# Kernel optimization log

Hardware: AMD Instinct MI355X
Metric: run time of the kernel (lower is better)

The kernel has to match this reference:

```python
import jax, jax.numpy as jnp
import numpy as np

D_MODEL = 1024
N_HEADS = 16
D_K = D_MODEL // N_HEADS


def setup_inputs() -> dict:
    key = jax.random.key(0)
    ks = jax.random.split(key, 11)
    B, S = 2, 2048
    s = 1.0 / np.sqrt(D_MODEL)
    return {
        "Q": jax.random.normal(ks[0], (B, S, D_MODEL), jnp.float32),
        "K": jax.random.normal(ks[1], (B, S, D_MODEL), jnp.float32),
        "V": jax.random.normal(ks[2], (B, S, D_MODEL), jnp.float32),
        "Wq": jax.random.normal(ks[3], (D_MODEL, D_MODEL), jnp.float32) * s,
        "bq": jnp.zeros((D_MODEL,), jnp.float32),
        "Wk": jax.random.normal(ks[4], (D_MODEL, D_MODEL), jnp.float32) * s,
        "bk": jnp.zeros((D_MODEL,), jnp.float32),
        "Wv": jax.random.normal(ks[5], (D_MODEL, D_MODEL), jnp.float32) * s,
        "bv": jnp.zeros((D_MODEL,), jnp.float32),
        "Wo": jax.random.normal(ks[6], (D_MODEL, D_MODEL), jnp.float32) * s,
        "bo": jnp.zeros((D_MODEL,), jnp.float32),
    }


def reference(Q, K, V, Wq, bq, Wk, bk, Wv, bv, Wo, bo):
    B, S, _ = Q.shape
    # linear projections (torch Linear: x @ W.T + b), split into heads
    def proj(x, W, b):
        y = x @ W.T + b                          # [B,S,D]
        return y.reshape(B, -1, N_HEADS, D_K).transpose(0, 2, 1, 3)  # [B,H,S,d_k]
    q = proj(Q, Wq, bq)
    k = proj(K, Wk, bk)
    v = proj(V, Wv, bv)
    scale = 1.0 / jnp.sqrt(jnp.float32(D_K))
    scores = jnp.einsum('bhqd,bhkd->bhqk', q, k) * scale  # [B,H,S,S]
    attn = jax.nn.softmax(scores, axis=-1)
    out = jnp.einsum('bhqk,bhkd->bhqd', attn, v)          # [B,H,S,d_k]
    out = out.transpose(0, 2, 1, 3).reshape(B, S, N_HEADS * D_K)
    return out @ Wo.T + bo
```

## Files before the change

kernel.cpp:

```cpp
#include <hip/hip_runtime.h>
#include <hip/hip_bf16.h>
#include <math.h>

#define D_MODEL 1024
#define NH      16
#define DK      64
#define S_LEN   2048
#define BATCH   2
#define M_ROWS  4096

typedef _Float16 f16;
typedef _Float16 f16x4 __attribute__((ext_vector_type(4)));
typedef _Float16 f16x8 __attribute__((ext_vector_type(8)));
typedef float    f32x4 __attribute__((ext_vector_type(4)));

__global__ __launch_bounds__(256) void cvt_f32_to_f16(
    const float* __restrict__ a, const float* __restrict__ b,
    const float* __restrict__ c, const float* __restrict__ d,
    f16* __restrict__ oa, f16* __restrict__ ob,
    f16* __restrict__ oc, f16* __restrict__ od, int n8) {
    const int y = blockIdx.y;
    const float* s = (y == 0) ? a : (y == 1) ? b : (y == 2) ? c : d;
    f16* o        = (y == 0) ? oa : (y == 1) ? ob : (y == 2) ? oc : od;
    if (s == nullptr) return;
    const int i = blockIdx.x * 256 + threadIdx.x;
    if (i >= n8) return;
    const size_t e = (size_t)i * 8;
    const float4 v0 = *(const float4*)&s[e];
    const float4 v1 = *(const float4*)&s[e + 4];
    f16x8 r = {(f16)v0.x, (f16)v0.y, (f16)v0.z, (f16)v0.w,
               (f16)v1.x, (f16)v1.y, (f16)v1.z, (f16)v1.w};
    *(f16x8*)&o[e] = r;
}

__device__ __forceinline__ void stage16(const f16* g, f16* l) {
    __builtin_amdgcn_global_load_lds(
        (const __attribute__((address_space(1))) unsigned int*)g,
        (__attribute__((address_space(3))) unsigned int*)l, 16, 0, 0);
}

__device__ __forceinline__ void gemm_body(const f16* __restrict__ X, const f16* __restrict__ W,
                                          const float* __restrict__ bias, void* __restrict__ Yv,
                                          const int mode, const float oscale) {
    __shared__ f16 As[128 * 32];
    __shared__ f16 Bs[128 * 32];
    const int tid = threadIdx.x;
    const int lane = tid & 63;
    const int w  = tid >> 6;
    const int wm = w >> 1, wn = w & 1;
    const int l15 = lane & 15, lhi = lane >> 4;
    const int m0 = blockIdx.y * 128, n0 = blockIdx.x * 128;

    const int srow = tid >> 2;
    const int scol = (tid & 3) * 8;

    f32x4 acc[4][4] = {};

    for (int k0 = 0; k0 < D_MODEL; k0 += 32) {
        __syncthreads();
        stage16(&X[(size_t)(m0 + srow) * D_MODEL + k0 + scol],      &As[tid * 8]);
        stage16(&X[(size_t)(m0 + 64 + srow) * D_MODEL + k0 + scol], &As[2048 + tid * 8]);
        stage16(&W[(size_t)(n0 + srow) * D_MODEL + k0 + scol],      &Bs[tid * 8]);
        stage16(&W[(size_t)(n0 + 64 + srow) * D_MODEL + k0 + scol], &Bs[2048 + tid * 8]);
        __syncthreads();
        f16x8 af[4], bf[4];
#pragma unroll
        for (int mt = 0; mt < 4; ++mt) af[mt] = *(const f16x8*)&As[(wm * 64 + mt * 16 + l15) * 32 + lhi * 8];
#pragma unroll
        for (int nt = 0; nt < 4; ++nt) bf[nt] = *(const f16x8*)&Bs[(wn * 64 + nt * 16 + l15) * 32 + lhi * 8];
#pragma unroll
        for (int mt = 0; mt < 4; ++mt)
#pragma unroll
            for (int nt = 0; nt < 4; ++nt)
                acc[mt][nt] = __builtin_amdgcn_mfma_f32_16x16x32_f16(af[mt], bf[nt], acc[mt][nt], 0, 0, 0);
    }

#pragma unroll
    for (int mt = 0; mt < 4; ++mt)
#pragma unroll
        for (int nt = 0; nt < 4; ++nt) {
            const int n = n0 + wn * 64 + nt * 16 + l15;
            const float bn = bias[n];
#pragma unroll
            for (int r = 0; r < 4; ++r) {
                const int m = m0 + wm * 64 + mt * 16 + lhi * 4 + r;
                const float v = (acc[mt][nt][r] + bn) * oscale;
                if (mode == 0) {
                    ((f16*)Yv)[((((size_t)(m >> 11) * NH + (n >> 6)) * S_LEN) + (m & 2047)) * DK + (n & 63)] = (f16)v;
                } else if (mode == 1) {
                    ((f16*)Yv)[((((size_t)(m >> 11) * NH + (n >> 6)) * DK) + (n & 63)) * S_LEN + (m & 2047)] = (f16)v;
                } else {
                    ((float*)Yv)[(size_t)m * D_MODEL + n] = v;
                }
            }
        }
}

__global__ __launch_bounds__(256) void qkv_gemm(
    const f16* __restrict__ Xq, const f16* __restrict__ Xk, const f16* __restrict__ Xv,
    const f16* __restrict__ Wq, const f16* __restrict__ Wk, const f16* __restrict__ Wv,
    const float* __restrict__ bq, const float* __restrict__ bk, const float* __restrict__ bv,
    f16* __restrict__ qh, f16* __restrict__ kh, f16* __restrict__ vt) {
    const int z = blockIdx.z;
    const f16* X = (z == 0) ? Xq : (z == 1) ? Xk : Xv;
    const f16* W = (z == 0) ? Wq : (z == 1) ? Wk : Wv;
    const float* bias = (z == 0) ? bq : (z == 1) ? bk : bv;
    f16* Y = (z == 0) ? qh : (z == 1) ? kh : vt;
    gemm_body(X, W, bias, Y, (z == 2) ? 1 : 0, (z == 0) ? 0.125f : 1.0f);
}

__global__ __launch_bounds__(256) void out_gemm(const f16* __restrict__ X, const f16* __restrict__ W,
                                                const float* __restrict__ bias, float* __restrict__ Y) {
    gemm_body(X, W, bias, Y, 2, 1.0f);
}

__global__ __launch_bounds__(256) void flash_mfma(const f16* __restrict__ qh, const f16* __restrict__ kh,
                                                  const f16* __restrict__ vt, f16* __restrict__ ao) {
    __shared__ f16 Ks[64][72];
    __shared__ f16 Vs[64][72];

    const int tid = threadIdx.x;
    const int lane = tid & 63;
    const int w = tid >> 6;
    const int c = lane & 15;
    const int g = lane >> 4;
    const int qt = blockIdx.x, bh = blockIdx.y;
    const int b = bh >> 4, h = bh & 15;
    const int qrow0 = qt * 64 + w * 16;

    f16x8 bQ0, bQ1;
    {
        const f16* qp = qh + ((size_t)bh * S_LEN + qrow0 + c) * DK;
        bQ0 = *(const f16x8*)&qp[g * 8];
        bQ1 = *(const f16x8*)&qp[32 + g * 8];
    }

    f32x4 oa[4] = {};
    float m_run = -INFINITY;
    float l_run = 0.f;

    const int cr = tid >> 3;
    const int cs = (tid & 7) * 8;

    for (int kt = 0; kt < S_LEN / 64; ++kt) {
        __syncthreads();
        {
            const uint4 k0v = *(const uint4*)&kh[((size_t)bh * S_LEN + kt * 64 + cr) * DK + cs];
            const uint4 k1v = *(const uint4*)&kh[((size_t)bh * S_LEN + kt * 64 + cr + 32) * DK + cs];
            const uint4 v0v = *(const uint4*)&vt[((size_t)bh * DK + cr) * S_LEN + kt * 64 + cs];
            const uint4 v1v = *(const uint4*)&vt[((size_t)bh * DK + cr + 32) * S_LEN + kt * 64 + cs];
            *(uint4*)&Ks[cr][cs] = k0v;
            *(uint4*)&Ks[cr + 32][cs] = k1v;
            *(uint4*)&Vs[cr][cs] = v0v;
            *(uint4*)&Vs[cr + 32][cs] = v1v;
        }
        __syncthreads();

        f32x4 sc[4] = {};
#pragma unroll
        for (int nt = 0; nt < 4; ++nt) {
            const f16x8 ka = *(const f16x8*)&Ks[nt * 16 + c][g * 8];
            const f16x8 kb = *(const f16x8*)&Ks[nt * 16 + c][32 + g * 8];
            sc[nt] = __builtin_amdgcn_mfma_f32_16x16x32_f16(ka, bQ0, sc[nt], 0, 0, 0);
            sc[nt] = __builtin_amdgcn_mfma_f32_16x16x32_f16(kb, bQ1, sc[nt], 0, 0, 0);
        }

        float tmax = sc[0][0];
#pragma unroll
        for (int nt = 0; nt < 4; ++nt)
#pragma unroll
            for (int r = 0; r < 4; ++r) tmax = fmaxf(tmax, sc[nt][r]);
        tmax = fmaxf(tmax, __shfl_xor(tmax, 16));
        tmax = fmaxf(tmax, __shfl_xor(tmax, 32));
        const float mnew = fmaxf(m_run, tmax);
        const float fac = __expf(m_run - mnew);
        m_run = mnew;

        float e[4][4];
        float tsum = 0.f;
#pragma unroll
        for (int nt = 0; nt < 4; ++nt)
#pragma unroll
            for (int r = 0; r < 4; ++r) {
                e[nt][r] = __expf(sc[nt][r] - mnew);
                tsum += e[nt][r];
            }
        tsum += __shfl_xor(tsum, 16);
        tsum += __shfl_xor(tsum, 32);
        l_run = l_run * fac + tsum;

#pragma unroll
        for (int r = 0; r < 4; ++r) {
            const float fr = __shfl(fac, (lane & 48) + ((lane >> 4) & 3) * 4 + r);
            oa[0][r] *= fr; oa[1][r] *= fr; oa[2][r] *= fr; oa[3][r] *= fr;
        }

        const f16x8 aP0 = {(f16)e[0][0], (f16)e[0][1], (f16)e[0][2], (f16)e[0][3],
                           (f16)e[1][0], (f16)e[1][1], (f16)e[1][2], (f16)e[1][3]};
        const f16x8 aP1 = {(f16)e[2][0], (f16)e[2][1], (f16)e[2][2], (f16)e[2][3],
                           (f16)e[3][0], (f16)e[3][1], (f16)e[3][2], (f16)e[3][3]};

#pragma unroll
        for (int nt2 = 0; nt2 < 4; ++nt2) {
            union { f16x8 v; f16x4 q[2]; } b0, b1;
            b0.q[0] = *(const f16x4*)&Vs[nt2 * 16 + c][g * 4];
            b0.q[1] = *(const f16x4*)&Vs[nt2 * 16 + c][16 + g * 4];
            b1.q[0] = *(const f16x4*)&Vs[nt2 * 16 + c][32 + g * 4];
            b1.q[1] = *(const f16x4*)&Vs[nt2 * 16 + c][48 + g * 4];
            oa[nt2] = __builtin_amdgcn_mfma_f32_16x16x32_f16(aP0, b0.v, oa[nt2], 0, 0, 0);
            oa[nt2] = __builtin_amdgcn_mfma_f32_16x16x32_f16(aP1, b1.v, oa[nt2], 0, 0, 0);
        }
    }

    const float invc = 1.f / l_run;
#pragma unroll
    for (int r = 0; r < 4; ++r) {
        const float ir = __shfl(invc, (lane & 48) + ((lane >> 4) & 3) * 4 + r);
        const int srow = qrow0 + ((lane >> 4) & 3) * 4 + r;
#pragma unroll
        for (int nt2 = 0; nt2 < 4; ++nt2) {
            ao[((size_t)b * S_LEN + srow) * D_MODEL + h * DK + nt2 * 16 + c] = (f16)(oa[nt2][r] * ir);
        }
    }
}

extern "C" void kernel_launch(void* const* d_in, const int* in_sizes, int n_in,
                              void* d_out, int out_size, void* d_ws, size_t ws_size,
                              hipStream_t stream) {
    const float* Q  = (const float*)d_in[0];
    const float* K  = (const float*)d_in[1];
    const float* V  = (const float*)d_in[2];
    const float* Wq = (const float*)d_in[3];
    const float* bq = (const float*)d_in[4];
    const float* Wk = (const float*)d_in[5];
    const float* bk = (const float*)d_in[6];
    const float* Wv = (const float*)d_in[7];
    const float* bv = (const float*)d_in[8];
    const float* Wo = (const float*)d_in[9];
    const float* bo = (const float*)d_in[10];
    float* out = (float*)d_out;

    const size_t NELEM = (size_t)M_ROWS * D_MODEL;
    const size_t WELEM = (size_t)D_MODEL * D_MODEL;
    f16* Qf  = (f16*)d_ws;
    f16* Kf  = Qf + NELEM;
    f16* Vf  = Kf + NELEM;
    f16* Wqf = Vf + NELEM;
    f16* Wkf = Wqf + WELEM;
    f16* Wvf = Wkf + WELEM;
    f16* Wof = Wvf + WELEM;
    f16* qh  = Wof + WELEM;
    f16* kh  = qh + NELEM;
    f16* vtw = kh + NELEM;
    f16* aow = vtw + NELEM;

    cvt_f32_to_f16<<<dim3(2048, 3), 256, 0, stream>>>(Q, K, V, nullptr, Qf, Kf, Vf, nullptr,
                                                      (int)(NELEM / 8));
    cvt_f32_to_f16<<<dim3(512, 4), 256, 0, stream>>>(Wq, Wk, Wv, Wo, Wqf, Wkf, Wvf, Wof,
                                                     (int)(WELEM / 8));
    qkv_gemm<<<dim3(D_MODEL / 128, M_ROWS / 128, 3), 256, 0, stream>>>(
        Qf, Kf, Vf, Wqf, Wkf, Wvf, bq, bk, bv, qh, kh, vtw);
    flash_mfma<<<dim3(S_LEN / 64, BATCH * NH), 256, 0, stream>>>(qh, kh, vtw, aow);
    out_gemm<<<dim3(D_MODEL / 128, M_ROWS / 128), 256, 0, stream>>>(aow, Wof, bo, out);
}
```

Measured before the change: 279.5 us.

## Prefetch K/V tiles, lazy softmax rescale, exp2, permuted V layout, smaller out-GEMM tiles

Several changes at once. The flash kernel now register-prefetches the next K/V tile, skips the output rescale unless the running max rises by more than a threshold, and uses the raw v_exp_f32 instruction with log2e folded into the Q scale. It also raises wave priority around the MFMA sections. The V projection is computed transposed and written with a permuted sequence order so that flash can read V with single 16-byte LDS loads. The output GEMM switches to 64x128 tiles so more blocks launch. Lazy rescaling can let intermediate values grow up to 2^8 in fp16, which adds some precision risk.

```diff
diff --git a/kernel.cpp b/kernel.cpp
--- a/kernel.cpp
+++ b/kernel.cpp
@@ -10,9 +10,18 @@
 #define M_ROWS  4096
 
 typedef _Float16 f16;
-typedef _Float16 f16x4 __attribute__((ext_vector_type(4)));
 typedef _Float16 f16x8 __attribute__((ext_vector_type(8)));
 typedef float    f32x4 __attribute__((ext_vector_type(4)));
+
+__device__ __forceinline__ float exp2_fast(float x) {
+    float r;
+    asm("v_exp_f32 %0, %1" : "=v"(r) : "v"(x));
+    return r;
+}
+
+__device__ __forceinline__ int perm6(int k) {
+    return (k & 35) | ((k & 12) << 1) | ((k & 16) >> 2);
+}
 
 __global__ __launch_bounds__(256) void cvt_f32_to_f16(
     const float* __restrict__ a, const float* __restrict__ b,
@@ -39,11 +48,10 @@
         (__attribute__((address_space(3))) unsigned int*)l, 16, 0, 0);
 }
 
-__device__ __forceinline__ void gemm_body(const f16* __restrict__ X, const f16* __restrict__ W,
+__device__ __forceinline__ void gemm_body(f16* As, f16* Bs,
+                                          const f16* __restrict__ X, const f16* __restrict__ W,
                                           const float* __restrict__ bias, void* __restrict__ Yv,
                                           const int mode, const float oscale) {
-    __shared__ f16 As[128 * 32];
-    __shared__ f16 Bs[128 * 32];
     const int tid = threadIdx.x;
     const int lane = tid & 63;
     const int w  = tid >> 6;
@@ -87,11 +95,59 @@
                 const float v = (acc[mt][nt][r] + bn) * oscale;
                 if (mode == 0) {
                     ((f16*)Yv)[((((size_t)(m >> 11) * NH + (n >> 6)) * S_LEN) + (m & 2047)) * DK + (n & 63)] = (f16)v;
-                } else if (mode == 1) {
-                    ((f16*)Yv)[((((size_t)(m >> 11) * NH + (n >> 6)) * DK) + (n & 63)) * S_LEN + (m & 2047)] = (f16)v;
                 } else {
                     ((float*)Yv)[(size_t)m * D_MODEL + n] = v;
                 }
+            }
+        }
+}
+
+__device__ __forceinline__ void gemm_body_vswap(f16* As, f16* Bs,
+                                                const f16* __restrict__ X, const f16* __restrict__ W,
+                                                const float* __restrict__ bias, f16* __restrict__ vt) {
+    const int tid = threadIdx.x;
+    const int lane = tid & 63;
+    const int w  = tid >> 6;
+    const int wm = w >> 1, wn = w & 1;
+    const int l15 = lane & 15, lhi = lane >> 4;
+    const int m0 = blockIdx.y * 128, n0 = blockIdx.x * 128;
+
+    const int srow = tid >> 2;
+    const int scol = (tid & 3) * 8;
+
+    f32x4 acc[4][4] = {};
+
+    for (int k0 = 0; k0 < D_MODEL; k0 += 32) {
+        __syncthreads();
+        stage16(&X[(size_t)(m0 + srow) * D_MODEL + k0 + scol],      &As[tid * 8]);
+        stage16(&X[(size_t)(m0 + 64 + srow) * D_MODEL + k0 + scol], &As[2048 + tid * 8]);
+        stage16(&W[(size_t)(n0 + srow) * D_MODEL + k0 + scol],      &Bs[tid * 8]);
+        stage16(&W[(size_t)(n0 + 64 + srow) * D_MODEL + k0 + scol], &Bs[2048 + tid * 8]);
+        __syncthreads();
+        f16x8 af[4], bf[4];
+#pragma unroll
+        for (int at = 0; at < 4; ++at) af[at] = *(const f16x8*)&Bs[(wm * 64 + at * 16 + l15) * 32 + lhi * 8];
+#pragma unroll
+        for (int bt = 0; bt < 4; ++bt) bf[bt] = *(const f16x8*)&As[(wn * 64 + bt * 16 + l15) * 32 + lhi * 8];
+#pragma unroll
+        for (int at = 0; at < 4; ++at)
+#pragma unroll
+            for (int bt = 0; bt < 4; ++bt)
+                acc[at][bt] = __builtin_amdgcn_mfma_f32_16x16x32_f16(af[at], bf[bt], acc[at][bt], 0, 0, 0);
+    }
+
+#pragma unroll
+    for (int at = 0; at < 4; ++at)
+#pragma unroll
+        for (int bt = 0; bt < 4; ++bt) {
+            const int m = m0 + wn * 64 + bt * 16 + l15;
+            const int b = m >> 11, s = m & 2047;
+#pragma unroll
+            for (int r = 0; r < 4; ++r) {
+                const int n = n0 + wm * 64 + at * 16 + lhi * 4 + r;
+                const float v = acc[at][bt][r] + bias[n];
+                const int s2 = (s & ~63) | perm6(s & 63);
+                vt[(((size_t)b * NH + (n >> 6)) * DK + (n & 63)) * S_LEN + s2] = (f16)v;
             }
         }
 }
@@ -101,17 +157,63 @@
     const f16* __restrict__ Wq, const f16* __restrict__ Wk, const f16* __restrict__ Wv,
     const float* __restrict__ bq, const float* __restrict__ bk, const float* __restrict__ bv,
     f16* __restrict__ qh, f16* __restrict__ kh, f16* __restrict__ vt) {
+    __shared__ f16 As[128 * 32];
+    __shared__ f16 Bs[128 * 32];
     const int z = blockIdx.z;
-    const f16* X = (z == 0) ? Xq : (z == 1) ? Xk : Xv;
-    const f16* W = (z == 0) ? Wq : (z == 1) ? Wk : Wv;
-    const float* bias = (z == 0) ? bq : (z == 1) ? bk : bv;
-    f16* Y = (z == 0) ? qh : (z == 1) ? kh : vt;
-    gemm_body(X, W, bias, Y, (z == 2) ? 1 : 0, (z == 0) ? 0.125f : 1.0f);
+    if (z == 2) {
+        gemm_body_vswap(As, Bs, Xv, Wv, bv, vt);
+    } else if (z == 0) {
+        gemm_body(As, Bs, Xq, Wq, bq, qh, 0, 0.125f * 1.44269504f);
+    } else {
+        gemm_body(As, Bs, Xk, Wk, bk, kh, 0, 1.0f);
+    }
 }
 
 __global__ __launch_bounds__(256) void out_gemm(const f16* __restrict__ X, const f16* __restrict__ W,
                                                 const float* __restrict__ bias, float* __restrict__ Y) {
-    gemm_body(X, W, bias, Y, 2, 1.0f);
+    __shared__ f16 As[64 * 32];
+    __shared__ f16 Bs[128 * 32];
+    const int tid = threadIdx.x;
+    const int lane = tid & 63;
+    const int w  = tid >> 6;
+    const int l15 = lane & 15, lhi = lane >> 4;
+    const int m0 = blockIdx.y * 64, n0 = blockIdx.x * 128;
+
+    const int srow = tid >> 2;
+    const int scol = (tid & 3) * 8;
+
+    f32x4 acc[4][2] = {};
+
+    for (int k0 = 0; k0 < D_MODEL; k0 += 32) {
+        __syncthreads();
+        stage16(&X[(size_t)(m0 + srow) * D_MODEL + k0 + scol],      &As[tid * 8]);
+        stage16(&W[(size_t)(n0 + srow) * D_MODEL + k0 + scol],      &Bs[tid * 8]);
+        stage16(&W[(size_t)(n0 + 64 + srow) * D_MODEL + k0 + scol], &Bs[2048 + tid * 8]);
+        __syncthreads();
+        f16x8 af[4], bf[2];
+#pragma unroll
+        for (int mt = 0; mt < 4; ++mt) af[mt] = *(const f16x8*)&As[(mt * 16 + l15) * 32 + lhi * 8];
+#pragma unroll
+        for (int nt = 0; nt < 2; ++nt) bf[nt] = *(const f16x8*)&Bs[(w * 32 + nt * 16 + l15) * 32 + lhi * 8];
+#pragma unroll
+        for (int mt = 0; mt < 4; ++mt)
+#pragma unroll
+            for (int nt = 0; nt < 2; ++nt)
+                acc[mt][nt] = __builtin_amdgcn_mfma_f32_16x16x32_f16(af[mt], bf[nt], acc[mt][nt], 0, 0, 0);
+    }
+
+#pragma unroll
+    for (int mt = 0; mt < 4; ++mt)
+#pragma unroll
+        for (int nt = 0; nt < 2; ++nt) {
+            const int n = n0 + w * 32 + nt * 16 + l15;
+            const float bn = bias[n];
+#pragma unroll
+            for (int r = 0; r < 4; ++r) {
+                const int m = m0 + mt * 16 + lhi * 4 + r;
+                Y[(size_t)m * D_MODEL + n] = acc[mt][nt][r] + bn;
+            }
+        }
 }
 
 __global__ __launch_bounds__(256) void flash_mfma(const f16* __restrict__ qh, const f16* __restrict__ kh,
@@ -142,21 +244,31 @@
     const int cr = tid >> 3;
     const int cs = (tid & 7) * 8;
 
+    const f16* kbase = kh + (size_t)bh * S_LEN * DK;
+    const f16* vbase = vt + (size_t)bh * DK * S_LEN;
+
+    uint4 kA = *(const uint4*)&kbase[(size_t)(cr) * DK + cs];
+    uint4 kB = *(const uint4*)&kbase[(size_t)(cr + 32) * DK + cs];
+    uint4 vA = *(const uint4*)&vbase[(size_t)cr * S_LEN + cs];
+    uint4 vB = *(const uint4*)&vbase[(size_t)(cr + 32) * S_LEN + cs];
+
     for (int kt = 0; kt < S_LEN / 64; ++kt) {
         __syncthreads();
-        {
-            const uint4 k0v = *(const uint4*)&kh[((size_t)bh * S_LEN + kt * 64 + cr) * DK + cs];
-            const uint4 k1v = *(const uint4*)&kh[((size_t)bh * S_LEN + kt * 64 + cr + 32) * DK + cs];
-            const uint4 v0v = *(const uint4*)&vt[((size_t)bh * DK + cr) * S_LEN + kt * 64 + cs];
-            const uint4 v1v = *(const uint4*)&vt[((size_t)bh * DK + cr + 32) * S_LEN + kt * 64 + cs];
-            *(uint4*)&Ks[cr][cs] = k0v;
-            *(uint4*)&Ks[cr + 32][cs] = k1v;
-            *(uint4*)&Vs[cr][cs] = v0v;
-            *(uint4*)&Vs[cr + 32][cs] = v1v;
+        *(uint4*)&Ks[cr][cs]      = kA;
+        *(uint4*)&Ks[cr + 32][cs] = kB;
+        *(uint4*)&Vs[cr][cs]      = vA;
+        *(uint4*)&Vs[cr + 32][cs] = vB;
+        if (kt + 1 < S_LEN / 64) {
+            const int o = (kt + 1) * 64;
+            kA = *(const uint4*)&kbase[(size_t)(o + cr) * DK + cs];
+            kB = *(const uint4*)&kbase[(size_t)(o + cr + 32) * DK + cs];
+            vA = *(const uint4*)&vbase[(size_t)cr * S_LEN + o + cs];
+            vB = *(const uint4*)&vbase[(size_t)(cr + 32) * S_LEN + o + cs];
         }
         __syncthreads();
 
         f32x4 sc[4] = {};
+        __builtin_amdgcn_s_setprio(1);
 #pragma unroll
         for (int nt = 0; nt < 4; ++nt) {
             const f16x8 ka = *(const f16x8*)&Ks[nt * 16 + c][g * 8];
@@ -164,6 +276,7 @@
             sc[nt] = __builtin_amdgcn_mfma_f32_16x16x32_f16(ka, bQ0, sc[nt], 0, 0, 0);
             sc[nt] = __builtin_amdgcn_mfma_f32_16x16x32_f16(kb, bQ1, sc[nt], 0, 0, 0);
         }
+        __builtin_amdgcn_s_setprio(0);
 
         float tmax = sc[0][0];
 #pragma unroll
@@ -172,9 +285,18 @@
             for (int r = 0; r < 4; ++r) tmax = fmaxf(tmax, sc[nt][r]);
         tmax = fmaxf(tmax, __shfl_xor(tmax, 16));
         tmax = fmaxf(tmax, __shfl_xor(tmax, 32));
-        const float mnew = fmaxf(m_run, tmax);
-        const float fac = __expf(m_run - mnew);
-        m_run = mnew;
+
+        if (!__all(tmax <= m_run + 8.f)) {
+            const float mnew = fmaxf(m_run, tmax);
+            const float fac = exp2_fast(m_run - mnew);
+            m_run = mnew;
+            l_run *= fac;
+#pragma unroll
+            for (int r = 0; r < 4; ++r) {
+                const float fr = __shfl(fac, (lane & 48) + ((lane >> 4) & 3) * 4 + r);
+                oa[0][r] *= fr; oa[1][r] *= fr; oa[2][r] *= fr; oa[3][r] *= fr;
+            }
+        }
 
         float e[4][4];
         float tsum = 0.f;
@@ -182,34 +304,27 @@
         for (int nt = 0; nt < 4; ++nt)
 #pragma unroll
             for (int r = 0; r < 4; ++r) {
-                e[nt][r] = __expf(sc[nt][r] - mnew);
+                e[nt][r] = exp2_fast(sc[nt][r] - m_run);
                 tsum += e[nt][r];
             }
         tsum += __shfl_xor(tsum, 16);
         tsum += __shfl_xor(tsum, 32);
-        l_run = l_run * fac + tsum;
-
-#pragma unroll
-        for (int r = 0; r < 4; ++r) {
-            const float fr = __shfl(fac, (lane & 48) + ((lane >> 4) & 3) * 4 + r);
-            oa[0][r] *= fr; oa[1][r] *= fr; oa[2][r] *= fr; oa[3][r] *= fr;
-        }
+        l_run += tsum;
 
         const f16x8 aP0 = {(f16)e[0][0], (f16)e[0][1], (f16)e[0][2], (f16)e[0][3],
                            (f16)e[1][0], (f16)e[1][1], (f16)e[1][2], (f16)e[1][3]};
         const f16x8 aP1 = {(f16)e[2][0], (f16)e[2][1], (f16)e[2][2], (f16)e[2][3],
                            (f16)e[3][0], (f16)e[3][1], (f16)e[3][2], (f16)e[3][3]};
 
+        __builtin_amdgcn_s_setprio(1);
 #pragma unroll
         for (int nt2 = 0; nt2 < 4; ++nt2) {
-            union { f16x8 v; f16x4 q[2]; } b0, b1;
-            b0.q[0] = *(const f16x4*)&Vs[nt2 * 16 + c][g * 4];
-            b0.q[1] = *(const f16x4*)&Vs[nt2 * 16 + c][16 + g * 4];
-            b1.q[0] = *(const f16x4*)&Vs[nt2 * 16 + c][32 + g * 4];
-            b1.q[1] = *(const f16x4*)&Vs[nt2 * 16 + c][48 + g * 4];
-            oa[nt2] = __builtin_amdgcn_mfma_f32_16x16x32_f16(aP0, b0.v, oa[nt2], 0, 0, 0);
-            oa[nt2] = __builtin_amdgcn_mfma_f32_16x16x32_f16(aP1, b1.v, oa[nt2], 0, 0, 0);
-        }
+            const f16x8 b0 = *(const f16x8*)&Vs[nt2 * 16 + c][g * 8];
+            const f16x8 b1 = *(const f16x8*)&Vs[nt2 * 16 + c][32 + g * 8];
+            oa[nt2] = __builtin_amdgcn_mfma_f32_16x16x32_f16(aP0, b0, oa[nt2], 0, 0, 0);
+            oa[nt2] = __builtin_amdgcn_mfma_f32_16x16x32_f16(aP1, b1, oa[nt2], 0, 0, 0);
+        }
+        __builtin_amdgcn_s_setprio(0);
     }
 
     const float invc = 1.f / l_run;
@@ -261,5 +376,5 @@
     qkv_gemm<<<dim3(D_MODEL / 128, M_ROWS / 128, 3), 256, 0, stream>>>(
         Qf, Kf, Vf, Wqf, Wkf, Wvf, bq, bk, bv, qh, kh, vtw);
     flash_mfma<<<dim3(S_LEN / 64, BATCH * NH), 256, 0, stream>>>(qh, kh, vtw, aow);
-    out_gemm<<<dim3(D_MODEL / 128, M_ROWS / 128), 256, 0, stream>>>(aow, Wof, bo, out);
-}
+    out_gemm<<<dim3(D_MODEL / 128, M_ROWS / 64), 256, 0, stream>>>(aow, Wof, bo, out);
+}
```

New measurement: 251.5 us. 1.11x faster.
